# Performance work log

Hardware: AMD Instinct MI355X
Metric: run time of the kernel (lower is better)

The kernel has to match this reference:

```python
import jax, jax.numpy as jnp
import numpy as np

N_NODES = 50000
N_EDGES = 800000
NODE_DIM = 256
HIDDEN_DIM = 256
LN_EPS = 1e-5


def setup_inputs() -> dict:
    key = jax.random.key(0)
    ks = jax.random.split(key, 8)
    d, h = NODE_DIM, HIDDEN_DIM
    return {
        "node_features": jax.random.normal(ks[0], (N_NODES, d), jnp.float32),
        "src": jax.random.randint(ks[1], (N_EDGES,), 0, N_NODES, jnp.int32),
        "dst": jax.random.randint(ks[2], (N_EDGES,), 0, N_NODES, jnp.int32),
        "edge_weight": jax.random.uniform(ks[3], (N_EDGES,), jnp.float32),
        "W1": jax.random.normal(ks[4], (d, h), jnp.float32) / np.sqrt(d),
        "b1": jnp.zeros((h,), jnp.float32),
        "g1": jnp.ones((h,), jnp.float32),
        "be1": jnp.zeros((h,), jnp.float32),
        "W2": jax.random.normal(ks[5], (h, h), jnp.float32) / np.sqrt(h),
        "b2": jnp.zeros((h,), jnp.float32),
        "g2": jnp.ones((h,), jnp.float32),
        "be2": jnp.zeros((h,), jnp.float32),
        "Wp": jax.random.normal(ks[6], (h, d), jnp.float32) / np.sqrt(h),
        "bp": jnp.zeros((d,), jnp.float32),
    }


def _spmm(src, dst, w, x, n):
    # sparse adj @ x : agg[i] = sum_{edges e with dst=i} w_e * x[src_e]
    return jax.ops.segment_sum(w[:, None] * x[src], dst, num_segments=n)


def _layer_norm(x, g, b):
    mu = jnp.mean(x, -1, keepdims=True)
    var = jnp.mean(jnp.square(x - mu), -1, keepdims=True)
    return (x - mu) * jax.lax.rsqrt(var + LN_EPS) * g + b


def reference(node_features, src, dst, edge_weight, W1, b1, g1, be1, W2, b2, g2, be2, Wp, bp):
    n = node_features.shape[0]
    x = node_features
    for (W, b, g, be) in ((W1, b1, g1, be1), (W2, b2, g2, be2)):
        agg = _spmm(src, dst, edge_weight, x, n)
        h = (x + agg) @ W + b
        x = jax.nn.gelu(_layer_norm(h, g, be), approximate=False)
        # Dropout(0.1) is identity in eval mode
    return x @ Wp + bp
```

## Files before the change

kernel.cpp:

```cpp
#include <hip/hip_runtime.h>
#include <hip/hip_bf16.h>
#include <math.h>

#define N_NODES 50000
#define N_EDGES 800000
#define DIM 256
#define MPAD 50176
#define LN_EPS 1e-5f
#define SCAN_BLOCKS 196

typedef short bf16x8 __attribute__((ext_vector_type(8)));
typedef float f32x16 __attribute__((ext_vector_type(16)));
typedef unsigned short u16;
typedef u16 u16x8 __attribute__((ext_vector_type(8)));

__device__ __forceinline__ u16 f2bf(float f) {
    union { float f; unsigned u; } v; v.f = f;
    unsigned r = (v.u + 0x7FFFu + ((v.u >> 16) & 1u)) >> 16;
    return (u16)r;
}
__device__ __forceinline__ float bf2f(u16 h) {
    union { unsigned u; float f; } v; v.u = ((unsigned)h) << 16;
    return v.f;
}
__device__ __forceinline__ float gelu_f(float x) {
    float z = x * (1.595769122f + 0.0713548162726f * x * x);
    return x * (1.0f / (1.0f + __expf(-z)));
}

__global__ void count_kernel(const int* __restrict__ dst, int* __restrict__ counts) {
    int e = blockIdx.x * 256 + threadIdx.x;
    if (e < N_EDGES) atomicAdd(&counts[dst[e]], 1);
}

__global__ void scan1_kernel(const int* __restrict__ counts, int* __restrict__ offsets,
                             int* __restrict__ bsum) {
    __shared__ int sh[256];
    int t = threadIdx.x;
    int idx = blockIdx.x * 256 + t;
    int v = (idx < N_NODES) ? counts[idx] : 0;
    sh[t] = v;
    __syncthreads();
#pragma unroll
    for (int off = 1; off < 256; off <<= 1) {
        int u = (t >= off) ? sh[t - off] : 0;
        __syncthreads();
        sh[t] += u;
        __syncthreads();
    }
    if (idx < N_NODES) offsets[idx] = sh[t] - v;
    if (t == 255) bsum[blockIdx.x] = sh[255];
}

__global__ void scan2_kernel(const int* __restrict__ bsum, int* __restrict__ bbase) {
    __shared__ int sh[256];
    int t = threadIdx.x;
    int v = (t < SCAN_BLOCKS) ? bsum[t] : 0;
    sh[t] = v;
    __syncthreads();
#pragma unroll
    for (int off = 1; off < 256; off <<= 1) {
        int u = (t >= off) ? sh[t - off] : 0;
        __syncthreads();
        sh[t] += u;
        __syncthreads();
    }
    if (t < SCAN_BLOCKS) bbase[t] = sh[t] - v;
}

__global__ void scan3_kernel(int* __restrict__ offsets, const int* __restrict__ bbase,
                             int* __restrict__ cursor) {
    int idx = blockIdx.x * 256 + threadIdx.x;
    if (idx < N_NODES) {
        int o = offsets[idx] + bbase[blockIdx.x];
        offsets[idx] = o;
        cursor[idx] = o;
    }
    if (idx == 0) offsets[N_NODES] = N_EDGES;
}

__global__ void scatter_kernel(const int* __restrict__ src, const int* __restrict__ dst,
                               const float* __restrict__ w, int* __restrict__ cursor,
                               int* __restrict__ sperm, float* __restrict__ wperm) {
    int e = blockIdx.x * 256 + threadIdx.x;
    if (e < N_EDGES) {
        int d = dst[e];
        int p = atomicAdd(&cursor[d], 1);
        sperm[p] = src[e];
        wperm[p] = w[e];
    }
}

__global__ void conv_kernel(const float* __restrict__ in, u16* __restrict__ out) {
    int i = blockIdx.x * 256 + threadIdx.x;
    float4 v = ((const float4*)in)[i];
    ushort4 o;
    o.x = f2bf(v.x); o.y = f2bf(v.y); o.z = f2bf(v.z); o.w = f2bf(v.w);
    ((ushort4*)out)[i] = o;
}

__global__ void convw_kernel(const float* __restrict__ W1, const float* __restrict__ W2,
                             const float* __restrict__ Wp, u16* __restrict__ WT) {
    int idx = blockIdx.x * 256 + threadIdx.x;
    int m = idx >> 16;
    int r = idx & 65535;
    int n = r >> 8, k = r & 255;
    const float* W = (m == 0) ? W1 : (m == 1) ? W2 : Wp;
    WT[idx] = f2bf(W[k * 256 + n]);
}

__global__ __launch_bounds__(256) void spmm_kernel(
        const u16* __restrict__ x, const int* __restrict__ offs,
        const int* __restrict__ sperm, const float* __restrict__ wperm,
        u16* __restrict__ y) {
    __shared__ u16 tile[32 * 264];
    int tid = threadIdx.x;
    int wave = tid >> 6;
    int lane = tid & 63;
    int node0 = blockIdx.x * 32 + wave * 8;

    const ushort4* xv = (const ushort4*)x;
#pragma unroll 1
    for (int i = 0; i < 8; ++i) {
        int node = node0 + i;
        float a0 = 0, a1 = 0, a2 = 0, a3 = 0;
        float b0 = 0, b1 = 0, b2 = 0, b3 = 0;
        float c0 = 0, c1 = 0, c2 = 0, c3 = 0;
        float d0 = 0, d1 = 0, d2 = 0, d3 = 0;
        if (node < N_NODES) {
            ushort4 v = xv[(size_t)node * 64 + lane];
            a0 = bf2f(v.x); a1 = bf2f(v.y); a2 = bf2f(v.z); a3 = bf2f(v.w);
            int p = offs[node];
            int p1 = offs[node + 1];
            for (; p + 4 <= p1; p += 4) {
                int s0 = sperm[p], s1 = sperm[p + 1], s2 = sperm[p + 2], s3 = sperm[p + 3];
                float w0 = wperm[p], w1 = wperm[p + 1], w2 = wperm[p + 2], w3 = wperm[p + 3];
                ushort4 v0 = xv[(size_t)s0 * 64 + lane];
                ushort4 v1 = xv[(size_t)s1 * 64 + lane];
                ushort4 v2 = xv[(size_t)s2 * 64 + lane];
                ushort4 v3 = xv[(size_t)s3 * 64 + lane];
                a0 += w0 * bf2f(v0.x); a1 += w0 * bf2f(v0.y); a2 += w0 * bf2f(v0.z); a3 += w0 * bf2f(v0.w);
                b0 += w1 * bf2f(v1.x); b1 += w1 * bf2f(v1.y); b2 += w1 * bf2f(v1.z); b3 += w1 * bf2f(v1.w);
                c0 += w2 * bf2f(v2.x); c1 += w2 * bf2f(v2.y); c2 += w2 * bf2f(v2.z); c3 += w2 * bf2f(v2.w);
                d0 += w3 * bf2f(v3.x); d1 += w3 * bf2f(v3.y); d2 += w3 * bf2f(v3.z); d3 += w3 * bf2f(v3.w);
            }
            for (; p < p1; ++p) {
                int s = sperm[p];
                float w = wperm[p];
                ushort4 vv = xv[(size_t)s * 64 + lane];
                a0 += w * bf2f(vv.x); a1 += w * bf2f(vv.y); a2 += w * bf2f(vv.z); a3 += w * bf2f(vv.w);
            }
            a0 += b0 + c0 + d0; a1 += b1 + c1 + d1;
            a2 += b2 + c2 + d2; a3 += b3 + c3 + d3;
        }
        ushort4 o;
        o.x = f2bf(a0); o.y = f2bf(a1); o.z = f2bf(a2); o.w = f2bf(a3);
        ((ushort4*)&tile[(wave * 8 + i) * 264])[lane] = o;
    }
    __syncthreads();
    u16* outb = y + (size_t)blockIdx.x * 8192;
#pragma unroll
    for (int hh = 0; hh < 4; ++hh) {
        int gi = tid + hh * 256;
        int kb = gi >> 6;
        int rem = gi & 63;
        int hf = rem >> 5, m = rem & 31;
        u16x8 v = *(const u16x8*)&tile[m * 264 + kb * 16 + hf * 8];
        *(u16x8*)(outb + (size_t)gi * 8) = v;
    }
}

template <int MODE, int OUT_TILED>
__global__ __launch_bounds__(256, 1) void gemm_kernel(
        const u16* __restrict__ A, const u16* __restrict__ BT,
        const float* __restrict__ bias, const float* __restrict__ g,
        const float* __restrict__ be, u16* __restrict__ xb_out,
        float* __restrict__ f_out) {
    __shared__ u16 b_lds[128 * 520];
    int tid = threadIdx.x;
    int wave = tid >> 6, lane = tid & 63;
    int l31 = lane & 31, half = lane >> 5;

#pragma unroll 8
    for (int i = 0; i < 32; ++i) {
        int s = i * 256 + tid;
        u16x8 v = *(const u16x8*)(BT + (size_t)s * 8);
        int n = s >> 5, kc = s & 31;
        int t = n >> 5, n32 = n & 31, kb = kc >> 1, hf = kc & 1;
        *(u16x8*)&b_lds[(t * 16 + kb) * 520 + hf * 256 + n32 * 8] = v;
    }

    int tile0 = blockIdx.x * 8 + wave * 2;
    const u16* ga0 = A + (size_t)tile0 * 8192 + lane * 8;
    const u16* ga1 = ga0 + 8192;
    bf16x8 p0 = *(const bf16x8*)ga0;
    bf16x8 p1 = *(const bf16x8*)ga1;

    f32x16 acc[2][8];
#pragma unroll
    for (int rf = 0; rf < 2; ++rf)
#pragma unroll
        for (int t = 0; t < 8; ++t)
#pragma unroll
            for (int r = 0; r < 16; ++r) acc[rf][t][r] = 0.f;

    __syncthreads();

#pragma unroll
    for (int kb = 0; kb < 16; ++kb) {
        bf16x8 a0 = p0, a1 = p1;
        if (kb < 15) {
            p0 = *(const bf16x8*)(ga0 + (kb + 1) * 512);
            p1 = *(const bf16x8*)(ga1 + (kb + 1) * 512);
        }
        const u16* bl = &b_lds[kb * 520 + lane * 8];
#pragma unroll
        for (int t = 0; t < 8; ++t) {
            bf16x8 bf = *(const bf16x8*)(bl + t * 16 * 520);
            acc[0][t] = __builtin_amdgcn_mfma_f32_32x32x16_bf16(a0, bf, acc[0][t], 0, 0, 0);
            acc[1][t] = __builtin_amdgcn_mfma_f32_32x32x16_bf16(a1, bf, acc[1][t], 0, 0, 0);
        }
    }

    float bv[8];
#pragma unroll
    for (int t = 0; t < 8; ++t) bv[t] = bias[t * 32 + l31];

#pragma unroll
    for (int rf = 0; rf < 2; ++rf) {
        int tile = tile0 + rf;
        if (MODE == 0) {
            float gv[8], bev[8];
#pragma unroll
            for (int t = 0; t < 8; ++t) {
                int c = t * 32 + l31;
                gv[t] = g[c]; bev[t] = be[c];
            }
#pragma unroll
            for (int r = 0; r < 16; ++r) {
                float s = 0.f, q = 0.f;
#pragma unroll
                for (int t = 0; t < 8; ++t) {
                    float v = acc[rf][t][r] + bv[t];
                    acc[rf][t][r] = v;
                    s += v; q += v * v;
                }
                for (int off = 1; off < 32; off <<= 1) {
                    s += __shfl_xor(s, off);
                    q += __shfl_xor(q, off);
                }
                float mu = s * (1.0f / 256.0f);
                float var = q * (1.0f / 256.0f) - mu * mu;
                float rs = rsqrtf(var + LN_EPS);
                int m = (r & 3) + 8 * (r >> 2) + 4 * half;
                int row = tile * 32 + m;
#pragma unroll
                for (int t = 0; t < 8; ++t) {
                    int c = t * 32 + l31;
                    float v = (acc[rf][t][r] - mu) * rs * gv[t] + bev[t];
                    u16 ob = f2bf(gelu_f(v));
                    if (OUT_TILED) {
                        size_t o = (size_t)tile * 8192 +
                                   ((size_t)(c >> 4) * 64 + ((c >> 3) & 1) * 32 + m) * 8 + (c & 7);
                        xb_out[o] = ob;
                    } else {
                        xb_out[(size_t)row * 256 + c] = ob;
                    }
                }
            }
        } else {
#pragma unroll
            for (int r = 0; r < 16; ++r) {
                int m = (r & 3) + 8 * (r >> 2) + 4 * half;
                int row = tile * 32 + m;
                if (row < N_NODES) {
#pragma unroll
                    for (int t = 0; t < 8; ++t) {
                        int c = t * 32 + l31;
                        f_out[(size_t)row * 256 + c] = acc[rf][t][r] + bv[t];
                    }
                }
            }
        }
    }
}

extern "C" void kernel_launch(void* const* d_in, const int* in_sizes, int n_in,
                              void* d_out, int out_size, void* d_ws, size_t ws_size,
                              hipStream_t stream) {
    const float* nodef = (const float*)d_in[0];
    const int*   src   = (const int*)d_in[1];
    const int*   dst   = (const int*)d_in[2];
    const float* ew    = (const float*)d_in[3];
    const float* W1 = (const float*)d_in[4];
    const float* b1 = (const float*)d_in[5];
    const float* g1 = (const float*)d_in[6];
    const float* be1 = (const float*)d_in[7];
    const float* W2 = (const float*)d_in[8];
    const float* b2 = (const float*)d_in[9];
    const float* g2 = (const float*)d_in[10];
    const float* be2 = (const float*)d_in[11];
    const float* Wp = (const float*)d_in[12];
    const float* bp = (const float*)d_in[13];
    float* out = (float*)d_out;

    char* ws = (char*)d_ws;
    size_t off = 0;
    auto alloc = [&](size_t bytes) -> void* {
        void* p = ws + off;
        off += (bytes + 255) & ~(size_t)255;
        return p;
    };
    u16*   ybuf    = (u16*)alloc((size_t)MPAD * 256 * 2);
    u16*   xbuf    = (u16*)alloc((size_t)MPAD * 256 * 2);
    u16*   WT      = (u16*)alloc((size_t)3 * 65536 * 2);
    int*   counts  = (int*)alloc((size_t)N_NODES * 4);
    int*   offsets = (int*)alloc((size_t)(N_NODES + 1) * 4);
    int*   cursor  = (int*)alloc((size_t)N_NODES * 4);
    int*   sperm   = (int*)alloc((size_t)N_EDGES * 4);
    float* wperm   = (float*)alloc((size_t)N_EDGES * 4);
    int*   bsum    = (int*)alloc((size_t)SCAN_BLOCKS * 4);
    int*   bbase   = (int*)alloc((size_t)SCAN_BLOCKS * 4);

    hipMemsetAsync(counts, 0, (size_t)N_NODES * 4, stream);
    count_kernel<<<(N_EDGES + 255) / 256, 256, 0, stream>>>(dst, counts);
    scan1_kernel<<<SCAN_BLOCKS, 256, 0, stream>>>(counts, offsets, bsum);
    scan2_kernel<<<1, 256, 0, stream>>>(bsum, bbase);
    scan3_kernel<<<SCAN_BLOCKS, 256, 0, stream>>>(offsets, bbase, cursor);
    scatter_kernel<<<(N_EDGES + 255) / 256, 256, 0, stream>>>(src, dst, ew, cursor, sperm, wperm);
    conv_kernel<<<N_NODES * 64 / 256, 256, 0, stream>>>(nodef, xbuf);
    convw_kernel<<<768, 256, 0, stream>>>(W1, W2, Wp, WT);

    const int GB = MPAD / 256;
    const int SB = MPAD / 32;
    spmm_kernel<<<SB, 256, 0, stream>>>(xbuf, offsets, sperm, wperm, ybuf);
    gemm_kernel<0, 0><<<GB, 256, 0, stream>>>(ybuf, WT, b1, g1, be1, xbuf, nullptr);
    spmm_kernel<<<SB, 256, 0, stream>>>(xbuf, offsets, sperm, wperm, ybuf);
    gemm_kernel<0, 1><<<GB, 256, 0, stream>>>(ybuf, WT + 65536, b2, g2, be2, ybuf, nullptr);
    gemm_kernel<1, 0><<<GB, 256, 0, stream>>>(ybuf, WT + 2 * 65536, bp, nullptr, nullptr, nullptr, out);
}
```

Before: 449.6 us.

## Pack edge src/weight pairs and split SpMM rows across half-waves

Edge source indices and weights are interleaved into one int2 array, so each edge needs one 8-byte load instead of two separate loads. The SpMM kernel now has each half-wave gather a full 512-byte row with 16-byte loads, the two halves handle alternating edges, and their partial sums are combined with a cross-lane shuffle. The LDS tile transpose is dropped: the kernel writes directly in the tiled layout the GEMM expects, and it launches twice as many blocks of 16 nodes each. The direct stores are narrower and less coalesced than the old staged write, and an odd leftover edge leaves half the wave idle.

```diff
diff --git a/kernel.cpp b/kernel.cpp
--- a/kernel.cpp
+++ b/kernel.cpp
@@ -81,13 +81,13 @@
 
 __global__ void scatter_kernel(const int* __restrict__ src, const int* __restrict__ dst,
                                const float* __restrict__ w, int* __restrict__ cursor,
-                               int* __restrict__ sperm, float* __restrict__ wperm) {
+                               int2* __restrict__ ep) {
     int e = blockIdx.x * 256 + threadIdx.x;
     if (e < N_EDGES) {
         int d = dst[e];
         int p = atomicAdd(&cursor[d], 1);
-        sperm[p] = src[e];
-        wperm[p] = w[e];
+        int2 v; v.x = src[e]; v.y = __float_as_int(w[e]);
+        ep[p] = v;
     }
 }
 
@@ -111,62 +111,67 @@
 
 __global__ __launch_bounds__(256) void spmm_kernel(
         const u16* __restrict__ x, const int* __restrict__ offs,
-        const int* __restrict__ sperm, const float* __restrict__ wperm,
-        u16* __restrict__ y) {
-    __shared__ u16 tile[32 * 264];
+        const int2* __restrict__ ep, u16* __restrict__ y) {
     int tid = threadIdx.x;
     int wave = tid >> 6;
     int lane = tid & 63;
-    int node0 = blockIdx.x * 32 + wave * 8;
-
-    const ushort4* xv = (const ushort4*)x;
+    int l31 = lane & 31, half = lane >> 5;
+    int node0 = blockIdx.x * 16 + wave * 4;
+
+    const u16x8* xv = (const u16x8*)x;
 #pragma unroll 1
-    for (int i = 0; i < 8; ++i) {
+    for (int i = 0; i < 4; ++i) {
         int node = node0 + i;
-        float a0 = 0, a1 = 0, a2 = 0, a3 = 0;
-        float b0 = 0, b1 = 0, b2 = 0, b3 = 0;
-        float c0 = 0, c1 = 0, c2 = 0, c3 = 0;
-        float d0 = 0, d1 = 0, d2 = 0, d3 = 0;
+        float acc[8];
+#pragma unroll
+        for (int j = 0; j < 8; ++j) acc[j] = 0.f;
         if (node < N_NODES) {
-            ushort4 v = xv[(size_t)node * 64 + lane];
-            a0 = bf2f(v.x); a1 = bf2f(v.y); a2 = bf2f(v.z); a3 = bf2f(v.w);
+            if (half == 0) {
+                u16x8 sv = xv[(size_t)node * 32 + l31];
+#pragma unroll
+                for (int j = 0; j < 8; ++j) acc[j] = bf2f(sv[j]);
+            }
             int p = offs[node];
             int p1 = offs[node + 1];
             for (; p + 4 <= p1; p += 4) {
-                int s0 = sperm[p], s1 = sperm[p + 1], s2 = sperm[p + 2], s3 = sperm[p + 3];
-                float w0 = wperm[p], w1 = wperm[p + 1], w2 = wperm[p + 2], w3 = wperm[p + 3];
-                ushort4 v0 = xv[(size_t)s0 * 64 + lane];
-                ushort4 v1 = xv[(size_t)s1 * 64 + lane];
-                ushort4 v2 = xv[(size_t)s2 * 64 + lane];
-                ushort4 v3 = xv[(size_t)s3 * 64 + lane];
-                a0 += w0 * bf2f(v0.x); a1 += w0 * bf2f(v0.y); a2 += w0 * bf2f(v0.z); a3 += w0 * bf2f(v0.w);
-                b0 += w1 * bf2f(v1.x); b1 += w1 * bf2f(v1.y); b2 += w1 * bf2f(v1.z); b3 += w1 * bf2f(v1.w);
-                c0 += w2 * bf2f(v2.x); c1 += w2 * bf2f(v2.y); c2 += w2 * bf2f(v2.z); c3 += w2 * bf2f(v2.w);
-                d0 += w3 * bf2f(v3.x); d1 += w3 * bf2f(v3.y); d2 += w3 * bf2f(v3.z); d3 += w3 * bf2f(v3.w);
-            }
-            for (; p < p1; ++p) {
-                int s = sperm[p];
-                float w = wperm[p];
-                ushort4 vv = xv[(size_t)s * 64 + lane];
-                a0 += w * bf2f(vv.x); a1 += w * bf2f(vv.y); a2 += w * bf2f(vv.z); a3 += w * bf2f(vv.w);
-            }
-            a0 += b0 + c0 + d0; a1 += b1 + c1 + d1;
-            a2 += b2 + c2 + d2; a3 += b3 + c3 + d3;
-        }
-        ushort4 o;
-        o.x = f2bf(a0); o.y = f2bf(a1); o.z = f2bf(a2); o.w = f2bf(a3);
-        ((ushort4*)&tile[(wave * 8 + i) * 264])[lane] = o;
-    }
-    __syncthreads();
-    u16* outb = y + (size_t)blockIdx.x * 8192;
-#pragma unroll
-    for (int hh = 0; hh < 4; ++hh) {
-        int gi = tid + hh * 256;
-        int kb = gi >> 6;
-        int rem = gi & 63;
-        int hf = rem >> 5, m = rem & 31;
-        u16x8 v = *(const u16x8*)&tile[m * 264 + kb * 16 + hf * 8];
-        *(u16x8*)(outb + (size_t)gi * 8) = v;
+                int2 e0 = ep[p + half];
+                int2 e1 = ep[p + 2 + half];
+                int s0 = e0.x; float w0 = __int_as_float(e0.y);
+                int s1 = e1.x; float w1 = __int_as_float(e1.y);
+                u16x8 v0 = xv[(size_t)s0 * 32 + l31];
+                u16x8 v1 = xv[(size_t)s1 * 32 + l31];
+#pragma unroll
+                for (int j = 0; j < 8; ++j) acc[j] += w0 * bf2f(v0[j]);
+#pragma unroll
+                for (int j = 0; j < 8; ++j) acc[j] += w1 * bf2f(v1[j]);
+            }
+            if (p + 2 <= p1) {
+                int2 e0 = ep[p + half];
+                int s0 = e0.x; float w0 = __int_as_float(e0.y);
+                u16x8 v0 = xv[(size_t)s0 * 32 + l31];
+#pragma unroll
+                for (int j = 0; j < 8; ++j) acc[j] += w0 * bf2f(v0[j]);
+                p += 2;
+            }
+            if (p < p1) {
+                int2 e0 = ep[p];
+                int s0 = e0.x;
+                float w0 = half ? 0.f : __int_as_float(e0.y);
+                u16x8 v0 = xv[(size_t)s0 * 32 + l31];
+#pragma unroll
+                for (int j = 0; j < 8; ++j) acc[j] += w0 * bf2f(v0[j]);
+            }
+        }
+#pragma unroll
+        for (int j = 0; j < 8; ++j) acc[j] += __shfl_xor(acc[j], 32);
+        if (half == 0) {
+            u16x8 o;
+#pragma unroll
+            for (int j = 0; j < 8; ++j) o[j] = f2bf(acc[j]);
+            int tile = node >> 5, m = node & 31;
+            int gi = (l31 >> 1) * 64 + (l31 & 1) * 32 + m;
+            *(u16x8*)(y + (size_t)tile * 8192 + (size_t)gi * 8) = o;
+        }
     }
 }
 
@@ -317,8 +322,7 @@
     int*   counts  = (int*)alloc((size_t)N_NODES * 4);
     int*   offsets = (int*)alloc((size_t)(N_NODES + 1) * 4);
     int*   cursor  = (int*)alloc((size_t)N_NODES * 4);
-    int*   sperm   = (int*)alloc((size_t)N_EDGES * 4);
-    float* wperm   = (float*)alloc((size_t)N_EDGES * 4);
+    int2*  ep      = (int2*)alloc((size_t)N_EDGES * 8);
     int*   bsum    = (int*)alloc((size_t)SCAN_BLOCKS * 4);
     int*   bbase   = (int*)alloc((size_t)SCAN_BLOCKS * 4);
 
@@ -327,15 +331,15 @@
     scan1_kernel<<<SCAN_BLOCKS, 256, 0, stream>>>(counts, offsets, bsum);
     scan2_kernel<<<1, 256, 0, stream>>>(bsum, bbase);
     scan3_kernel<<<SCAN_BLOCKS, 256, 0, stream>>>(offsets, bbase, cursor);
-    scatter_kernel<<<(N_EDGES + 255) / 256, 256, 0, stream>>>(src, dst, ew, cursor, sperm, wperm);
+    scatter_kernel<<<(N_EDGES + 255) / 256, 256, 0, stream>>>(src, dst, ew, cursor, ep);
     conv_kernel<<<N_NODES * 64 / 256, 256, 0, stream>>>(nodef, xbuf);
     convw_kernel<<<768, 256, 0, stream>>>(W1, W2, Wp, WT);
 
     const int GB = MPAD / 256;
-    const int SB = MPAD / 32;
-    spmm_kernel<<<SB, 256, 0, stream>>>(xbuf, offsets, sperm, wperm, ybuf);
+    const int SB = MPAD / 16;
+    spmm_kernel<<<SB, 256, 0, stream>>>(xbuf, offsets, ep, ybuf);
     gemm_kernel<0, 0><<<GB, 256, 0, stream>>>(ybuf, WT, b1, g1, be1, xbuf, nullptr);
-    spmm_kernel<<<SB, 256, 0, stream>>>(xbuf, offsets, sperm, wperm, ybuf);
+    spmm_kernel<<<SB, 256, 0, stream>>>(xbuf, offsets, ep, ybuf);
     gemm_kernel<0, 1><<<GB, 256, 0, stream>>>(ybuf, WT + 65536, b2, g2, be2, ybuf, nullptr);
     gemm_kernel<1, 0><<<GB, 256, 0, stream>>>(ybuf, WT + 2 * 65536, bp, nullptr, nullptr, nullptr, out);
 }
```

Result: slower. 478.3 us (+6.4%).
